# Kernel optimization log

Hardware: AMD Instinct MI355X
Metric: run time of the kernel (lower is better)

Reference implementation:

```python
import jax, jax.numpy as jnp
import numpy as np

B, S, D, H = 4, 2048, 1024, 16
DK = D // H

def setup_inputs() -> dict:
    key = jax.random.key(0)
    ks = jax.random.split(key, 8)
    q = jax.random.normal(ks[0], (B, S, D), dtype=jnp.float32)
    k = jax.random.normal(ks[1], (B, S, D), dtype=jnp.float32)
    v = jax.random.normal(ks[2], (B, S, D), dtype=jnp.float32)
    # broadcastable causal mask [1,1,S,S]; 0 -> masked
    mask = jnp.tril(jnp.ones((S, S), dtype=jnp.int32))[None, None]
    sc = 1.0 / np.sqrt(D)
    w_q = jax.random.normal(ks[3], (D, D), dtype=jnp.float32) * sc
    w_k = jax.random.normal(ks[4], (D, D), dtype=jnp.float32) * sc
    w_v = jax.random.normal(ks[5], (D, D), dtype=jnp.float32) * sc
    w_o = jax.random.normal(ks[6], (D, D), dtype=jnp.float32) * sc
    return {"q": q, "k": k, "v": v, "mask": mask,
            "w_q": w_q, "w_k": w_k, "w_v": w_v, "w_o": w_o}


def reference(q, k, v, mask, w_q, w_k, w_v, w_o):
    # Linear (no bias): x @ W^T, torch convention
    def proj(x, w):
        return jnp.einsum('bsd,ed->bse', x, w)
    # [B,S,D] -> [B,H,S,DK]
    def split_heads(x):
        return x.reshape(B, S, H, DK).transpose(0, 2, 1, 3)

    query = split_heads(proj(q, w_q))
    key_ = split_heads(proj(k, w_k))
    value = split_heads(proj(v, w_v))

    scores = jnp.einsum('bhqd,bhkd->bhqk', query, key_) / jnp.sqrt(
        jnp.asarray(DK, dtype=query.dtype))
    scores = jnp.where(mask == 0, jnp.asarray(-1e9, dtype=scores.dtype), scores)
    attn = jax.nn.softmax(scores, axis=-1)  # dropout p=0.0 -> identity
    x = jnp.einsum('bhqk,bhkd->bhqd', attn, value)
    x = x.transpose(0, 2, 1, 3).reshape(B, S, D)
    return jnp.einsum('bsd,ed->bse', x, w_o)
```

## Files before the change

kernel.cpp:

```cpp
#include <hip/hip_runtime.h>
#include <hip/hip_bf16.h>

#define B_ 4
#define S_ 2048
#define D_ 1024
#define H_ 16
#define DK_ 64

typedef unsigned short u16;
typedef __bf16 bf16x8 __attribute__((ext_vector_type(8)));
typedef float f32x4 __attribute__((ext_vector_type(4)));

typedef const unsigned int __attribute__((address_space(1))) guint;
typedef unsigned int __attribute__((address_space(3))) luint;

__device__ __forceinline__ void gld16(const u16* g, u16* l) {
  __builtin_amdgcn_global_load_lds((guint*)g, (luint*)l, 16, 0, 0);
}

__device__ __forceinline__ u16 f2b(float f) {
  __hip_bfloat16 h = __float2bfloat16(f);
  return __builtin_bit_cast(u16, h);
}
__device__ __forceinline__ ushort4 f2b4(float4 f) {
  ushort4 r;
  r.x = f2b(f.x); r.y = f2b(f.y); r.z = f2b(f.z); r.w = f2b(f.w);
  return r;
}
__device__ __forceinline__ bf16x8 ldb8(const u16* p) {
  union { uint4 u; bf16x8 v; } x;
  x.u = *(const uint4*)p;
  return x.v;
}

struct CvtAllArgs {
  const float* s[7];
  u16* d[7];
};
__global__ __launch_bounds__(256) void cvt_all(CvtAllArgs a) {
  const int z = blockIdx.y;
  const int bx = blockIdx.x;
  const float* s;
  u16* d;
  int i;
  if (z < 3) {
    s = a.s[z]; d = a.d[z];
    i = bx * 256 + threadIdx.x;
  } else {
    if (bx >= 2048) return;
    const int wsel = bx >> 9;
    s = a.s[3 + wsel]; d = a.d[3 + wsel];
    i = (bx & 511) * 256 + threadIdx.x;
  }
  float4 x = ((const float4*)s)[2 * i];
  float4 y = ((const float4*)s)[2 * i + 1];
  ((ushort4*)d)[2 * i] = f2b4(x);
  ((ushort4*)d)[2 * i + 1] = f2b4(y);
}

template <bool OUT_QKV>
__device__ __forceinline__ void gemm_body2(const u16* __restrict__ A,
                                           const u16* __restrict__ W,
                                           void* __restrict__ C, float scale,
                                           int bm, int bn) {
  constexpr int K = D_;
  constexpr int NS = K / 32;
  __shared__ u16 Ab[3 * 4096];
  __shared__ u16 Bb[3 * 8192];
  const int t = threadIdx.x;
  const int lane = t & 63, w = t >> 6;
  const int quad = lane >> 4, m16 = lane & 15;
  const int wm = w >> 2, wn = w & 3;

  int aoff[4], boff[4];
#pragma unroll
  for (int i = 0; i < 4; i++) {
    int a = (wm * 64 + i * 16 + m16) * 64 + quad * 16;
    a ^= ((a >> 7) & 3) << 4;
    aoff[i] = a >> 1;
    int bb = (wn * 64 + i * 16 + m16) * 64 + quad * 16;
    bb ^= ((bb >> 7) & 3) << 4;
    boff[i] = bb >> 1;
  }

  const int cs8 = ((t & 3) ^ ((t >> 3) & 3)) * 8;
  const u16* aps = A + (size_t)(bm * 128 + (t >> 2)) * K + cs8;
  const u16* bps0 = W + (size_t)(bn * 256 + (t >> 2)) * K + cs8;
  const u16* bps1 = W + (size_t)(bn * 256 + 128 + (t >> 2)) * K + cs8;
  const int wb = w * 512;

  f32x4 acc[4][4];
  const f32x4 zero = {0.f, 0.f, 0.f, 0.f};
#pragma unroll
  for (int i = 0; i < 4; i++)
#pragma unroll
    for (int j = 0; j < 4; j++) acc[i][j] = zero;

  gld16(aps, &Ab[wb]);
  gld16(bps0, &Bb[wb]);
  gld16(bps1, &Bb[4096 + wb]);
  gld16(aps + 32, &Ab[4096 + wb]);
  gld16(bps0 + 32, &Bb[8192 + wb]);
  gld16(bps1 + 32, &Bb[8192 + 4096 + wb]);
  aps += 64; bps0 += 64; bps1 += 64;
  asm volatile("s_waitcnt vmcnt(3)" ::: "memory");
  __builtin_amdgcn_s_barrier();
  __builtin_amdgcn_sched_barrier(0);

  int cb = 0, nb = 1, sb = 2;
#pragma unroll 1
  for (int s = 0; s < NS; s++) {
    const u16* Ac = &Ab[cb * 4096];
    const u16* Bc = &Bb[cb * 8192];
    const bool st = (s + 2 < NS);
    if (st) gld16(aps, &Ab[sb * 4096 + wb]);
    bf16x8 bf0 = ldb8(Bc + boff[0]);
    bf16x8 bf1 = ldb8(Bc + boff[1]);
    bf16x8 bf2 = ldb8(Bc + boff[2]);
    bf16x8 bf3 = ldb8(Bc + boff[3]);
    bf16x8 a0 = ldb8(Ac + aoff[0]);
    bf16x8 a1 = ldb8(Ac + aoff[1]);
    __builtin_amdgcn_s_setprio(1);
    acc[0][0] = __builtin_amdgcn_mfma_f32_16x16x32_bf16(a0, bf0, acc[0][0], 0, 0, 0);
    acc[0][1] = __builtin_amdgcn_mfma_f32_16x16x32_bf16(a0, bf1, acc[0][1], 0, 0, 0);
    acc[0][2] = __builtin_amdgcn_mfma_f32_16x16x32_bf16(a0, bf2, acc[0][2], 0, 0, 0);
    acc[0][3] = __builtin_amdgcn_mfma_f32_16x16x32_bf16(a0, bf3, acc[0][3], 0, 0, 0);
    acc[1][0] = __builtin_amdgcn_mfma_f32_16x16x32_bf16(a1, bf0, acc[1][0], 0, 0, 0);
    acc[1][1] = __builtin_amdgcn_mfma_f32_16x16x32_bf16(a1, bf1, acc[1][1], 0, 0, 0);
    acc[1][2] = __builtin_amdgcn_mfma_f32_16x16x32_bf16(a1, bf2, acc[1][2], 0, 0, 0);
    acc[1][3] = __builtin_amdgcn_mfma_f32_16x16x32_bf16(a1, bf3, acc[1][3], 0, 0, 0);
    __builtin_amdgcn_s_setprio(0);
    __builtin_amdgcn_s_barrier();
    if (st) {
      gld16(bps0, &Bb[sb * 8192 + wb]);
      gld16(bps1, &Bb[sb * 8192 + 4096 + wb]);
    }
    bf16x8 a2 = ldb8(Ac + aoff[2]);
    bf16x8 a3 = ldb8(Ac + aoff[3]);
    __builtin_amdgcn_s_setprio(1);
    acc[2][0] = __builtin_amdgcn_mfma_f32_16x16x32_bf16(a2, bf0, acc[2][0], 0, 0, 0);
    acc[2][1] = __builtin_amdgcn_mfma_f32_16x16x32_bf16(a2, bf1, acc[2][1], 0, 0, 0);
    acc[2][2] = __builtin_amdgcn_mfma_f32_16x16x32_bf16(a2, bf2, acc[2][2], 0, 0, 0);
    acc[2][3] = __builtin_amdgcn_mfma_f32_16x16x32_bf16(a2, bf3, acc[2][3], 0, 0, 0);
    acc[3][0] = __builtin_amdgcn_mfma_f32_16x16x32_bf16(a3, bf0, acc[3][0], 0, 0, 0);
    acc[3][1] = __builtin_amdgcn_mfma_f32_16x16x32_bf16(a3, bf1, acc[3][1], 0, 0, 0);
    acc[3][2] = __builtin_amdgcn_mfma_f32_16x16x32_bf16(a3, bf2, acc[3][2], 0, 0, 0);
    acc[3][3] = __builtin_amdgcn_mfma_f32_16x16x32_bf16(a3, bf3, acc[3][3], 0, 0, 0);
    __builtin_amdgcn_s_setprio(0);
    if (st) asm volatile("s_waitcnt vmcnt(3)" ::: "memory");
    else    asm volatile("s_waitcnt vmcnt(0)" ::: "memory");
    __builtin_amdgcn_sched_barrier(0);
    __builtin_amdgcn_s_barrier();
    __builtin_amdgcn_sched_barrier(0);
    aps += 32; bps0 += 32; bps1 += 32;
    int tmp = cb; cb = nb; nb = sb; sb = tmp;
  }

#pragma unroll
  for (int mi = 0; mi < 4; mi++) {
#pragma unroll
    for (int r = 0; r < 4; r++) {
      int m = bm * 128 + wm * 64 + mi * 16 + quad * 4 + r;
#pragma unroll
      for (int nf = 0; nf < 4; nf++) {
        int n = bn * 256 + wn * 64 + nf * 16 + m16;
        float val = acc[mi][nf][r] * scale;
        if (OUT_QKV) {
          int b = m >> 11, s = m & (S_ - 1);
          int h = n >> 6, dk = n & 63;
          ((u16*)C)[(((size_t)b * H_ + h) * S_ + s) * DK_ + dk] = f2b(val);
        } else {
          ((float*)C)[(size_t)m * D_ + n] = val;
        }
      }
    }
  }
}

struct GemmQkvArgs {
  const u16 *a0, *a1, *a2;
  const u16 *w0, *w1, *w2;
  u16 *c0, *c1, *c2;
  float qscale;
};
__global__ __launch_bounds__(512, 2) void gemm_qkv(GemmQkvArgs g) {
  const int id3 = (blockIdx.z * 64 + blockIdx.y) * 4 + blockIdx.x;
  const int wgn = (id3 & 7) * 96 + (id3 >> 3);
  const int zz = wgn >> 8, rem = wgn & 255;
  const int bm = rem >> 2, bn = rem & 3;
  const u16* A = zz == 0 ? g.a0 : zz == 1 ? g.a1 : g.a2;
  const u16* W = zz == 0 ? g.w0 : zz == 1 ? g.w1 : g.w2;
  u16* C = zz == 0 ? g.c0 : zz == 1 ? g.c1 : g.c2;
  gemm_body2<true>(A, W, C, zz == 0 ? g.qscale : 1.0f, bm, bn);
}

__global__ __launch_bounds__(512, 2) void gemm_o(const u16* __restrict__ A,
                                                 const u16* __restrict__ W,
                                                 float* __restrict__ C) {
  const int id2 = blockIdx.y * 4 + blockIdx.x;
  const int wgn = (id2 & 7) * 32 + (id2 >> 3);
  const int bm = wgn >> 2, bn = wgn & 3;
  gemm_body2<false>(A, W, C, 1.0f, bm, bn);
}

__global__ __launch_bounds__(256) void transpose_v(const u16* __restrict__ Vp,
                                                   u16* __restrict__ VpT) {
  constexpr int LDT = 72;
  __shared__ u16 T[64 * LDT];
  const int t = threadIdx.x;
  const int s0 = blockIdx.x * 64, bh = blockIdx.y;
  const size_t base = (size_t)bh * S_ * DK_;
  const int rot = t & 7;
#pragma unroll
  for (int i = 0; i < 2; i++) {
    int c = t + i * 256, row = c >> 3, c8 = (c & 7) * 8;
    union { uint4 u; u16 s[8]; } uv;
    uv.u = *(const uint4*)(Vp + base + (size_t)(s0 + row) * DK_ + c8);
#pragma unroll
    for (int j0 = 0; j0 < 8; j0++) {
      int j = (j0 + rot) & 7;
      T[(c8 + j) * LDT + row] = uv.s[j];
    }
  }
  __syncthreads();
#pragma unroll
  for (int i = 0; i < 2; i++) {
    int c = t + i * 256, row = c >> 3, c8 = (c & 7) * 8;
    uint4 val = *(const uint4*)&T[row * LDT + c8];
    *(uint4*)(VpT + base + (size_t)row * S_ + s0 + c8) = val;
  }
}

__global__ __launch_bounds__(512, 4) void flash_attn(const u16* __restrict__ Qp,
                                                     const u16* __restrict__ Kp,
                                                     const u16* __restrict__ VpT,
                                                     u16* __restrict__ Xb) {
  constexpr int LDK = 72;
  __shared__ u16 Ks[2][64 * LDK];
  __shared__ u16 Vt[2][64 * LDK];
  __shared__ u16 Ps[8][16 * LDK];
  const int t = threadIdx.x;
  const int lane = t & 63, w = t >> 6;
  const int quad = lane >> 4, m16 = lane & 15;
  const int id = blockIdx.x;
  const int g = (id >> 3) & 7;
  const int bh = (id & 7) * 8 + (id >> 6);
  const int b = bh >> 4, h = bh & (H_ - 1);
  const size_t base = (size_t)bh * S_ * DK_;
  const int srow = t >> 3, sc8 = (t & 7) * 8;
  const f32x4 zero = {0.f, 0.f, 0.f, 0.f};

#pragma unroll 1
  for (int pi = 0; pi < 2; pi++) {
    const int qt = pi ? (15 - g) : g;
    const int q0 = qt * 128;
    const int nT = 2 * qt + 2;

    const int qrow = q0 + w * 16 + m16;
    bf16x8 qf0 = ldb8(Qp + base + (size_t)qrow * DK_ + quad * 8);
    bf16x8 qf1 = ldb8(Qp + base + (size_t)qrow * DK_ + 32 + quad * 8);

    f32x4 acc[4];
#pragma unroll
    for (int i = 0; i < 4; i++) acc[i] = zero;
    float rsum[4] = {0.f, 0.f, 0.f, 0.f};

    uint4 kr = *(const uint4*)(Kp + base + (size_t)srow * DK_ + sc8);
    uint4 vr = *(const uint4*)(VpT + base + (size_t)srow * S_ + sc8);

#pragma unroll 1
    for (int ti = 0; ti < nT; ti++) {
      const int kt0 = ti * 64;
      const int cur = ti & 1;
      *(uint4*)&Ks[cur][srow * LDK + sc8] = kr;
      *(uint4*)&Vt[cur][srow * LDK + sc8] = vr;
      __syncthreads();
      if (ti + 1 < nT) {
        kr = *(const uint4*)(Kp + base + (size_t)(kt0 + 64 + srow) * DK_ + sc8);
        vr = *(const uint4*)(VpT + base + (size_t)srow * S_ + kt0 + 64 + sc8);
      }
      const u16* Kc = Ks[cur];
      const u16* Vc = Vt[cur];

      f32x4 sc[4];
      __builtin_amdgcn_s_setprio(1);
#pragma unroll
      for (int nt = 0; nt < 4; nt++) {
        bf16x8 kf0 = ldb8(&Kc[(nt * 16 + m16) * LDK + quad * 8]);
        bf16x8 kf1 = ldb8(&Kc[(nt * 16 + m16) * LDK + 32 + quad * 8]);
        sc[nt] = __builtin_amdgcn_mfma_f32_16x16x32_bf16(kf0, qf0, zero, 0, 0, 0);
        sc[nt] = __builtin_amdgcn_mfma_f32_16x16x32_bf16(kf1, qf1, sc[nt], 0, 0, 0);
      }
      __builtin_amdgcn_s_setprio(0);

      if (ti >= nT - 2) {
        const int qcol = q0 + w * 16 + m16;
#pragma unroll
        for (int nt = 0; nt < 4; nt++) {
          int kg = kt0 + nt * 16 + quad * 4;
#pragma unroll
          for (int r = 0; r < 4; r++)
            if (kg + r > qcol) sc[nt][r] = -1e30f;
        }
      }

      u16* Pw = &Ps[w][0];
#pragma unroll
      for (int nt = 0; nt < 4; nt++) {
        ushort4 pk;
        float p0 = __builtin_amdgcn_exp2f(sc[nt][0]);
        float p1 = __builtin_amdgcn_exp2f(sc[nt][1]);
        float p2 = __builtin_amdgcn_exp2f(sc[nt][2]);
        float p3 = __builtin_amdgcn_exp2f(sc[nt][3]);
        rsum[nt] += (p0 + p1) + (p2 + p3);
        pk.x = f2b(p0); pk.y = f2b(p1); pk.z = f2b(p2); pk.w = f2b(p3);
        *(ushort4*)&Pw[m16 * LDK + nt * 16 + quad * 4] = pk;
      }

      __builtin_amdgcn_s_setprio(1);
#pragma unroll
      for (int s2 = 0; s2 < 2; s2++) {
        bf16x8 pf = ldb8(&Pw[m16 * LDK + s2 * 32 + quad * 8]);
#pragma unroll
        for (int nt = 0; nt < 4; nt++) {
          bf16x8 vf = ldb8(&Vc[(nt * 16 + m16) * LDK + s2 * 32 + quad * 8]);
          acc[nt] = __builtin_amdgcn_mfma_f32_16x16x32_bf16(pf, vf, acc[nt], 0, 0, 0);
        }
      }
      __builtin_amdgcn_s_setprio(0);
    }

    float tot = (rsum[0] + rsum[1]) + (rsum[2] + rsum[3]);
    tot += __shfl_xor(tot, 16);
    tot += __shfl_xor(tot, 32);
    float rcv[4];
#pragma unroll
    for (int r = 0; r < 4; r++)
      rcv[r] = __builtin_amdgcn_rcpf(__shfl(tot, quad * 4 + r, 16));
#pragma unroll
    for (int nt = 0; nt < 4; nt++)
#pragma unroll
      for (int r = 0; r < 4; r++) {
        int rg = q0 + w * 16 + quad * 4 + r;
        Xb[((size_t)b * S_ + rg) * D_ + h * DK_ + nt * 16 + m16] =
            f2b(acc[nt][r] * rcv[r]);
      }
  }
}

extern "C" void kernel_launch(void* const* d_in, const int* in_sizes, int n_in,
                              void* d_out, int out_size, void* d_ws, size_t ws_size,
                              hipStream_t stream) {
  (void)in_sizes; (void)n_in; (void)out_size; (void)ws_size;
  const float* q = (const float*)d_in[0];
  const float* k = (const float*)d_in[1];
  const float* v = (const float*)d_in[2];
  const float* wq = (const float*)d_in[4];
  const float* wk = (const float*)d_in[5];
  const float* wv = (const float*)d_in[6];
  const float* wo = (const float*)d_in[7];

  const size_t nBSD = (size_t)B_ * S_ * D_;
  const size_t nDD = (size_t)D_ * D_;
  u16* ab = (u16*)d_ws;
  u16* wqb = ab + nBSD;
  u16* wkb = wqb + nDD;
  u16* wvb = wkb + nDD;
  u16* wob = wvb + nDD;
  u16* Qp = wob + nDD;
  u16* Kp = Qp + nBSD;
  u16* Vp = Kp + nBSD;
  u16* VpT = ab;
  u16* Xb = Vp;
  u16* abk = (u16*)d_out;
  u16* abv = abk + nBSD;

  const float qscale = 0.125f * 1.44269504089f;

  CvtAllArgs ca = {{q, k, v, wq, wk, wv, wo}, {ab, abk, abv, wqb, wkb, wvb, wob}};
  cvt_all<<<dim3(nBSD / 2048, 4), 256, 0, stream>>>(ca);

  GemmQkvArgs gq = {ab, abk, abv, wqb, wkb, wvb, Qp, Kp, Vp, qscale};
  gemm_qkv<<<dim3(4, 64, 3), 512, 0, stream>>>(gq);

  transpose_v<<<dim3(S_ / 64, B_ * H_), 256, 0, stream>>>(Vp, VpT);
  flash_attn<<<512, 512, 0, stream>>>(Qp, Kp, VpT, Xb);

  gemm_o<<<dim3(4, 64), 512, 0, stream>>>(Xb, wob, (float*)d_out);
}
```

Measured before the change: 327.1 us.

## Replace QKV projection GEMM with 256x256 tile, 8-wave ping-pong pipelined kernel

Adds a new QKV projection GEMM that uses 256x256 output tiles with K-step 64 and double-buffered LDS loaded via global_load_lds. It runs a hand-scheduled ping-pong loop that interleaves barriers, s_setprio and partial vmcnt waits so MFMA work overlaps with LDS fragment loads and global prefetches. The grid is halved and the old gemm_qkv kernel is removed. The larger tile raises reuse per block but needs 128KB of LDS and many accumulator registers, which may limit occupancy to one block per CU.

```diff
diff --git a/kernel.cpp b/kernel.cpp
--- a/kernel.cpp
+++ b/kernel.cpp
@@ -56,6 +56,154 @@
   float4 y = ((const float4*)s)[2 * i + 1];
   ((ushort4*)d)[2 * i] = f2b4(x);
   ((ushort4*)d)[2 * i + 1] = f2b4(y);
+}
+
+template <int MH, int NH>
+__device__ __forceinline__ void mm16(f32x4 (&acc)[8][4], const bf16x8* aA,
+                                     const bf16x8* bV) {
+#pragma unroll
+  for (int mi2 = 0; mi2 < 4; mi2++)
+#pragma unroll
+    for (int ni2 = 0; ni2 < 2; ni2++) {
+      f32x4 v = acc[MH * 4 + mi2][NH * 2 + ni2];
+      v = __builtin_amdgcn_mfma_f32_16x16x32_bf16(aA[mi2 * 2 + 0], bV[ni2 * 2 + 0], v, 0, 0, 0);
+      v = __builtin_amdgcn_mfma_f32_16x16x32_bf16(aA[mi2 * 2 + 1], bV[ni2 * 2 + 1], v, 0, 0, 0);
+      acc[MH * 4 + mi2][NH * 2 + ni2] = v;
+    }
+}
+
+#define BAR __builtin_amdgcn_s_barrier()
+#define PRIO1 __builtin_amdgcn_s_setprio(1)
+#define PRIO0 __builtin_amdgcn_s_setprio(0)
+#define STGA(b, h, tt)                                                         \
+  do {                                                                         \
+    gld16(Ag + (size_t)(h) * 128 * K + (size_t)(tt) * 64,                      \
+          &As[(b) * 16384 + (h) * 8192 + w * 512]);                            \
+    gld16(Ag + ((size_t)(h) * 128 + 64) * K + (size_t)(tt) * 64,               \
+          &As[(b) * 16384 + (h) * 8192 + 4096 + w * 512]);                     \
+  } while (0)
+#define STGB(b, h, tt)                                                         \
+  do {                                                                         \
+    gld16(Wg + (size_t)(h) * 128 * K + (size_t)(tt) * 64,                      \
+          &Bs[(b) * 16384 + (h) * 8192 + w * 512]);                            \
+    gld16(Wg + ((size_t)(h) * 128 + 64) * K + (size_t)(tt) * 64,               \
+          &Bs[(b) * 16384 + (h) * 8192 + 4096 + w * 512]);                     \
+  } while (0)
+#define LDA8(b, mh)                                                            \
+  do {                                                                         \
+    _Pragma("unroll") for (int q_ = 0; q_ < 8; q_++)                           \
+        aA[q_] = ldb8(&As[(b) * 16384 +                                        \
+            (((arb + ((mh) * 4 + (q_ >> 1)) * 2048 + (q_ & 1) * 64) ^ aswz) >> 1)]); \
+  } while (0)
+#define LDB4(b, nh, dst)                                                       \
+  do {                                                                         \
+    _Pragma("unroll") for (int q_ = 0; q_ < 4; q_++)                           \
+        dst[q_] = ldb8(&Bs[(b) * 16384 +                                       \
+            (((brb + ((nh) * 2 + (q_ >> 1)) * 2048 + (q_ & 1) * 64) ^ aswz) >> 1)]); \
+  } while (0)
+
+template <bool OUT_QKV>
+__device__ __forceinline__ void gemm8_body(const u16* __restrict__ A,
+                                           const u16* __restrict__ W,
+                                           void* __restrict__ C, float scale,
+                                           int bm, int bn) {
+  constexpr int K = D_;
+  constexpr int NI = 8;
+  __shared__ u16 As[2 * 16384];
+  __shared__ u16 Bs[2 * 16384];
+  const int t = threadIdx.x;
+  const int l = t & 63, w = t >> 6;
+  const int quad = l >> 4, m16 = l & 15;
+  const int wm = w >> 2, wn = w & 3;
+  const int lr = l >> 3;
+  const int aswz = (m16 & 7) << 4;
+
+  const u16* Ag = A + (size_t)(bm * 256 + w * 8 + lr) * K + ((l & 7) ^ lr) * 8;
+  const u16* Wg = W + (size_t)(bn * 256 + w * 8 + lr) * K + ((l & 7) ^ lr) * 8;
+  const int arb = (wm * 128 + m16) * 128 + quad * 16;
+  const int brb = (wn * 64 + m16) * 128 + quad * 16;
+
+  f32x4 acc[8][4];
+  const f32x4 zero = {0.f, 0.f, 0.f, 0.f};
+#pragma unroll
+  for (int i = 0; i < 8; i++)
+#pragma unroll
+    for (int j = 0; j < 4; j++) acc[i][j] = zero;
+
+  bf16x8 aA[8], b0v[4], b1v[4];
+
+  STGB(0, 0, 0); STGB(0, 1, 0); STGA(0, 0, 0); STGA(0, 1, 0);
+  STGB(1, 0, 1); STGB(1, 1, 1); STGA(1, 0, 1);
+  asm volatile("s_waitcnt vmcnt(6)" ::: "memory");
+  BAR;
+
+#pragma unroll 1
+  for (int j = 0; j < NI; j++) {
+    const int tb1 = 2 * j + 1, ta2 = 2 * j + 2, tb2 = 2 * j + 3;
+    const bool st = (j + 1 < NI);
+    STGA(1, 1, tb1);
+    LDA8(0, 0);
+    LDB4(0, 0, b0v);
+    BAR; PRIO1; mm16<0, 0>(acc, aA, b0v); PRIO0; BAR;
+    LDB4(0, 1, b1v);
+    BAR; PRIO1; mm16<0, 1>(acc, aA, b1v); PRIO0; BAR;
+    if (st) { STGB(0, 0, ta2); }
+    LDA8(0, 1);
+    BAR; PRIO1; mm16<1, 1>(acc, aA, b1v); PRIO0; BAR;
+    if (st) { STGB(0, 1, ta2); STGA(0, 0, ta2); }
+    if (st) asm volatile("s_waitcnt vmcnt(6)" ::: "memory");
+    else    asm volatile("s_waitcnt vmcnt(0)" ::: "memory");
+    BAR; PRIO1; mm16<1, 0>(acc, aA, b0v); PRIO0; BAR;
+    if (st) { STGA(0, 1, ta2); }
+    LDA8(1, 0);
+    LDB4(1, 0, b0v);
+    BAR; PRIO1; mm16<0, 0>(acc, aA, b0v); PRIO0; BAR;
+    LDB4(1, 1, b1v);
+    BAR; PRIO1; mm16<0, 1>(acc, aA, b1v); PRIO0; BAR;
+    if (st) { STGB(1, 0, tb2); }
+    LDA8(1, 1);
+    BAR; PRIO1; mm16<1, 1>(acc, aA, b1v); PRIO0; BAR;
+    if (st) { STGB(1, 1, tb2); STGA(1, 0, tb2); }
+    if (st) asm volatile("s_waitcnt vmcnt(6)" ::: "memory");
+    BAR; PRIO1; mm16<1, 0>(acc, aA, b0v); PRIO0; BAR;
+  }
+
+#pragma unroll
+  for (int mi = 0; mi < 8; mi++) {
+#pragma unroll
+    for (int r = 0; r < 4; r++) {
+      int m = bm * 256 + wm * 128 + mi * 16 + quad * 4 + r;
+#pragma unroll
+      for (int ni = 0; ni < 4; ni++) {
+        int n = bn * 256 + wn * 64 + ni * 16 + m16;
+        float val = acc[mi][ni][r] * scale;
+        if (OUT_QKV) {
+          int b = m >> 11, s = m & (S_ - 1);
+          int h = n >> 6, dk = n & 63;
+          ((u16*)C)[(((size_t)b * H_ + h) * S_ + s) * DK_ + dk] = f2b(val);
+        } else {
+          ((float*)C)[(size_t)m * D_ + n] = val;
+        }
+      }
+    }
+  }
+}
+
+struct GemmQkvArgs {
+  const u16 *a0, *a1, *a2;
+  const u16 *w0, *w1, *w2;
+  u16 *c0, *c1, *c2;
+  float qscale;
+};
+__global__ __launch_bounds__(512, 2) void gemm_qkv8(GemmQkvArgs g) {
+  const int id3 = (blockIdx.z * 32 + blockIdx.y) * 4 + blockIdx.x;
+  const int wg = (id3 & 7) * 48 + (id3 >> 3);
+  const int zz = wg >> 7, rem = wg & 127;
+  const int bm = rem >> 2, bn = rem & 3;
+  const u16* A = zz == 0 ? g.a0 : zz == 1 ? g.a1 : g.a2;
+  const u16* W = zz == 0 ? g.w0 : zz == 1 ? g.w1 : g.w2;
+  u16* C = zz == 0 ? g.c0 : zz == 1 ? g.c1 : g.c2;
+  gemm8_body<true>(A, W, C, zz == 0 ? g.qscale : 1.0f, bm, bn);
 }
 
 template <bool OUT_QKV>
@@ -177,23 +325,6 @@
   }
 }
 
-struct GemmQkvArgs {
-  const u16 *a0, *a1, *a2;
-  const u16 *w0, *w1, *w2;
-  u16 *c0, *c1, *c2;
-  float qscale;
-};
-__global__ __launch_bounds__(512, 2) void gemm_qkv(GemmQkvArgs g) {
-  const int id3 = (blockIdx.z * 64 + blockIdx.y) * 4 + blockIdx.x;
-  const int wgn = (id3 & 7) * 96 + (id3 >> 3);
-  const int zz = wgn >> 8, rem = wgn & 255;
-  const int bm = rem >> 2, bn = rem & 3;
-  const u16* A = zz == 0 ? g.a0 : zz == 1 ? g.a1 : g.a2;
-  const u16* W = zz == 0 ? g.w0 : zz == 1 ? g.w1 : g.w2;
-  u16* C = zz == 0 ? g.c0 : zz == 1 ? g.c1 : g.c2;
-  gemm_body2<true>(A, W, C, zz == 0 ? g.qscale : 1.0f, bm, bn);
-}
-
 __global__ __launch_bounds__(512, 2) void gemm_o(const u16* __restrict__ A,
                                                  const u16* __restrict__ W,
                                                  float* __restrict__ C) {
@@ -381,7 +512,7 @@
   cvt_all<<<dim3(nBSD / 2048, 4), 256, 0, stream>>>(ca);
 
   GemmQkvArgs gq = {ab, abk, abv, wqb, wkb, wvb, Qp, Kp, Vp, qscale};
-  gemm_qkv<<<dim3(4, 64, 3), 512, 0, stream>>>(gq);
+  gemm_qkv8<<<dim3(4, 32, 3), 512, 0, stream>>>(gq);
 
   transpose_v<<<dim3(S_ / 64, B_ * H_), 256, 0, stream>>>(Vp, VpT);
   flash_attn<<<512, 512, 0, stream>>>(Qp, Kp, VpT, Xb);
```

Result: slower. 335.2 us (+2.5%).
